# Kernel optimization log

Measured on AMD Instinct MI355X. Metric: run time of the kernel, lower is better.

## Reference

```python
import jax, jax.numpy as jnp
import numpy as np

B, N_NODES, T_IN = 512, 32, 12
HID, HEADS, OUT_CH, DEG = 64, 8, 9, 8


def setup_inputs() -> dict:
    key = jax.random.key(0)
    ks = jax.random.split(key, 26)
    rn = lambda k, s, sc=0.1: (jax.random.normal(k, s, jnp.float32) * sc)
    E = B * N_NODES * DEG
    src = jax.random.randint(ks[0], (E,), 0, N_NODES, jnp.int32)
    dst = jax.random.randint(ks[1], (E,), 0, N_NODES, jnp.int32)
    off = jnp.repeat(jnp.arange(B, dtype=jnp.int32) * N_NODES, N_NODES * DEG)
    edge_index = jnp.stack([src + off, dst + off])  # block-diagonal batched graph
    x = jax.random.normal(ks[2], (B, N_NODES, T_IN), jnp.float32)
    return {
        "x": x,
        "edge_index": edge_index,
        # gat1: in=T_IN -> HEADS*HID, concat
        "W1": rn(ks[3], (T_IN, HEADS * HID)),
        "a_src1": rn(ks[4], (HEADS, HID)),
        "a_dst1": rn(ks[5], (HEADS, HID)),
        "b1": rn(ks[6], (HEADS * HID,), 0.01),
        # gat2: in=HEADS*HID -> HID, heads=1, mean (concat=False)
        "W2": rn(ks[7], (HEADS * HID, HID), 0.05),
        "a_src2": rn(ks[8], (1, HID)),
        "a_dst2": rn(ks[9], (1, HID)),
        "b2": rn(ks[10], (HID,), 0.01),
        "gamma": jnp.ones((HID,), jnp.float32),
        "beta": jnp.zeros((HID,), jnp.float32),
        # gru1: input_size=N_NODES(=32), hidden=HID
        "Wi1": rn(ks[11], (3 * HID, N_NODES)),
        "Wh1": rn(ks[12], (3 * HID, HID)),
        "bi1": rn(ks[13], (3 * HID,), 0.01),
        "bh1": rn(ks[14], (3 * HID,), 0.01),
        # gru2: input_size=HID, hidden=HID
        "Wi2": rn(ks[15], (3 * HID, HID)),
        "Wh2": rn(ks[16], (3 * HID, HID)),
        "bi2": rn(ks[17], (3 * HID,), 0.01),
        "bh2": rn(ks[18], (3 * HID,), 0.01),
        "Wf": rn(ks[19], (OUT_CH, HID)),
        "bf": rn(ks[20], (OUT_CH,), 0.01),
    }


def _gat_layer(x, src, dst, W, a_s, a_d, b, concat):
    # PyG GATConv (eval mode, self-loops already appended by caller)
    Nn = x.shape[0]
    heads, hc = a_s.shape
    h = (x @ W).reshape(Nn, heads, hc)                 # [N, H, C]
    es = jnp.sum(h * a_s, axis=-1)                     # [N, H]
    ed = jnp.sum(h * a_d, axis=-1)
    e = jax.nn.leaky_relu(es[src] + ed[dst], 0.2)      # [E, H]
    m = jax.ops.segment_max(e, dst, num_segments=Nn)
    p = jnp.exp(e - m[dst])
    s = jax.ops.segment_sum(p, dst, num_segments=Nn)
    alpha = p / (s[dst] + 1e-16)                       # per-dst softmax
    out = jax.ops.segment_sum(h[src] * alpha[:, :, None], dst, num_segments=Nn)
    out = out.reshape(Nn, heads * hc) if concat else out.mean(axis=1)
    return out + b


def _gru(x, Wi, Wh, bi, bh):
    # torch.nn.GRU (batch_first) single layer; x: [B, T, F]
    H = Wh.shape[1]
    xi = x @ Wi.T + bi                                 # [B, T, 3H]
    def step(h, xt):
        gh = h @ Wh.T + bh
        r = jax.nn.sigmoid(xt[:, :H] + gh[:, :H])
        z = jax.nn.sigmoid(xt[:, H:2 * H] + gh[:, H:2 * H])
        n = jnp.tanh(xt[:, 2 * H:] + r * gh[:, 2 * H:])
        hn = (1.0 - z) * n + z * h
        return hn, hn
    h0 = jnp.zeros((x.shape[0], H), x.dtype)
    _, ys = jax.lax.scan(step, h0, jnp.swapaxes(xi, 0, 1))
    return jnp.swapaxes(ys, 0, 1)


def reference(x, edge_index, W1, a_src1, a_dst1, b1, W2, a_src2, a_dst2, b2,
              gamma, beta, Wi1, Wh1, bi1, bh1, Wi2, Wh2, bi2, bh2, Wf, bf):
    Bsz, Nn_, T = x.shape
    Nn = Bsz * Nn_
    xf = x.reshape(Nn, T)                              # dropout is identity in eval
    sl = jnp.arange(Nn, dtype=edge_index.dtype)        # PyG add_self_loops=True
    src = jnp.concatenate([edge_index[0], sl])
    dst = jnp.concatenate([edge_index[1], sl])
    h = jax.nn.elu(_gat_layer(xf, src, dst, W1, a_src1, a_dst1, b1, True))
    h = jax.nn.elu(_gat_layer(h, src, dst, W2, a_src2, a_dst2, b2, False))
    mu = h.mean(-1, keepdims=True)
    var = ((h - mu) ** 2).mean(-1, keepdims=True)
    h = (h - mu) / jnp.sqrt(var + 1e-5) * gamma + beta
    seq = h.reshape(Bsz, Nn_, -1).transpose(0, 2, 1)   # [B, HID(seq), N_NODES(feat)]
    g = _gru(seq, Wi1, Wh1, bi1, bh1)
    g = _gru(g, Wi2, Wh2, bi2, bh2)
    return g[:, -1, :] @ Wf.T + bf                     # [B, OUT_CH]
```

## Files before the change

### kernel.cpp

```cpp
#include <hip/hip_runtime.h>
#include <hip/hip_bf16.h>
#include <stdint.h>

#define BATCH 512
#define NN 32
#define T_IN 12
#define HID 64
#define HEADS 8
#define OUT_CH 9
#define EPB (NN*8)
#define ETOT (EPB+NN)
#define F1 (HEADS*HID)

using u16 = unsigned short;
using u32 = unsigned int;
typedef _Float16 f16;
typedef _Float16 f16x2 __attribute__((ext_vector_type(2)));
typedef u32 v4u __attribute__((ext_vector_type(4)));
typedef float v4f __attribute__((ext_vector_type(4)));

__device__ __forceinline__ float bf2f(u16 u){ return __uint_as_float(((u32)u)<<16); }
__device__ __forceinline__ u16 f2bf(float f){
    u32 x = __float_as_uint(f);
    u32 r = (x + 0x7FFFu + ((x>>16)&1u))>>16;
    return (u16)r;
}
__device__ __forceinline__ u32 packf16(float a, float b){
    f16x2 p; p.x=(f16)a; p.y=(f16)b; return __builtin_bit_cast(u32,p);
}
__device__ __forceinline__ u16 f2h16(float a){ f16 h=(f16)a; return __builtin_bit_cast(u16,h); }
__device__ __forceinline__ float h16f(u16 v){ f16 h=__builtin_bit_cast(f16,v); return (float)h; }
__device__ __forceinline__ float lof(u32 w){ return (float)__builtin_bit_cast(f16x2,w).x; }
__device__ __forceinline__ float hif(u32 w){ return (float)__builtin_bit_cast(f16x2,w).y; }
__device__ __forceinline__ float dot2(u32 a, u32 b, float c){
#if __has_builtin(__builtin_amdgcn_fdot2)
    return __builtin_amdgcn_fdot2(__builtin_bit_cast(f16x2,a), __builtin_bit_cast(f16x2,b), c, false);
#else
    return fmaf(lof(a),lof(b), fmaf(hif(a),hif(b), c));
#endif
}
__device__ __forceinline__ float elu1(float x){ return x > 0.f ? x : (__expf(x)-1.f); }
__device__ __forceinline__ float sigm(float x){ return 1.f/(1.f+__expf(-x)); }
__device__ __forceinline__ float tanh_(float x){ return 1.f - 2.f/(__expf(2.f*x)+1.f); }
__device__ __forceinline__ u32 fenc(float v){
    u32 b=__float_as_uint(v);
    return (b&0x80000000u) ? ~b : (b|0x80000000u);
}
__device__ __forceinline__ float fdec(u32 k){
    return __uint_as_float((k&0x80000000u) ? (k&0x7FFFFFFFu) : ~k);
}

#define DOT4(acc,A,W) do{ acc=dot2(A.x,W.x,acc); acc=dot2(A.y,W.y,acc); \
                          acc=dot2(A.z,W.z,acc); acc=dot2(A.w,W.w,acc); }while(0)
#define DOT32(acc,A0,A1,A2,A3,A4,A5,A6,A7,W0,W1,W2,W3,W4,W5,W6,W7) do{ \
    DOT4(acc,A0,W0); DOT4(acc,A1,W1); DOT4(acc,A2,W2); DOT4(acc,A3,W3); \
    DOT4(acc,A4,W4); DOT4(acc,A5,W5); DOT4(acc,A6,W6); DOT4(acc,A7,W7); }while(0)

__global__ __launch_bounds__(256) void k_detect(const u32* __restrict__ xw, int* __restrict__ flag){
    __shared__ int cnt;
    if(threadIdx.x==0) cnt=0;
    __syncthreads();
    int c=0;
    for(int i=threadIdx.x;i<4096;i+=256){
        u32 w=xw[i];
        if(w & 0x7FFFFFFFu){
            u32 el=(w>>7)&0xFFu;
            if(el>=0x90u) c++;
        }
    }
    atomicAdd(&cnt,c);
    __syncthreads();
    if(threadIdx.x==0) *flag = (cnt>256) ? 1 : 0;
}

struct CvtDesc {
    const void* src[16];
    void*       dst[16];
    int         n[16];
};

__global__ __launch_bounds__(256) void k_convert(CvtDesc d, const int* __restrict__ flag){
    const int seg = blockIdx.x;
    const int f = *flag;
    const void* s = d.src[seg];
    const int n = d.n[seg];
    const int stride = gridDim.y*256;
    float* o=(float*)d.dst[seg];
    for(int i=blockIdx.y*256+threadIdx.x;i<n;i+=stride)
        o[i] = f ? ((const float*)s)[i] : bf2f(((const u16*)s)[i]);
}

__global__ __launch_bounds__(256) void k_prep(
    const void* __restrict__ W2src, u16* __restrict__ W2i,
    const void* __restrict__ Wi1, const void* __restrict__ Wh1,
    const void* __restrict__ Wi2, const void* __restrict__ Wh2,
    u32* __restrict__ wpk, const int* __restrict__ flag)
{
    const int f=*flag;
    if(blockIdx.x<128){
        int i = blockIdx.x*256+threadIdx.x;
        int k=i>>6, j=i&63;
        float v = f? ((const float*)W2src)[i] : bf2f(((const u16*)W2src)[i]);
        W2i[ (((size_t)(k>>3)*64 + j)<<3) + (k&7) ] = f2h16(v);
    } else {
        int w = (blockIdx.x-128)*256+threadIdx.x;
        int m = w/6144;
        int rem = w - m*6144;
        int row = rem>>5, kw = rem&31;
        const void* s = (m==0)?Wi1 : (m==1)?Wh1 : (m==2)?Wi2 : Wh2;
        int K = (m==0)?32:64;
        int k0=2*kw, k1=k0+1;
        float v0=0.f, v1=0.f;
        if(k0<K) v0 = f? ((const float*)s)[row*K+k0] : bf2f(((const u16*)s)[row*K+k0]);
        if(k1<K) v1 = f? ((const float*)s)[row*K+k1] : bf2f(((const u16*)s)[row*K+k1]);
        wpk[w]=packf16(v0,v1);
    }
}

__global__ __launch_bounds__(256,2) void k_gat1(
    const float* __restrict__ x, const int* __restrict__ ei,
    const float* __restrict__ W1, const float* __restrict__ a_s, const float* __restrict__ a_d,
    const float* __restrict__ b1, u32* __restrict__ h1g)
{
    const int b = blockIdx.x, t = threadIdx.x;
    __shared__ __align__(16) float s_x[NN][12];
    __shared__ float s_W1[T_IN*F1];
    __shared__ __align__(16) u16 s_h[NN][520];
    __shared__ __align__(16) u32 s_aspk[HEADS*32], s_adpk[HEADS*32];
    __shared__ float s_es[NN][HEADS], s_ed[NN][HEADS];
    __shared__ unsigned char s_src[ETOT], s_dst[ETOT];
    __shared__ float s_al[HEADS][ETOT];
    __shared__ u32 s_mx[NN*HEADS];
    __shared__ float s_sm[NN*HEADS], s_inv[NN*HEADS];
    __shared__ int s_cnt[NN], s_off[NN], s_fil[NN];
    __shared__ short s_lst[ETOT];

    for(int i=t;i<NN*T_IN;i+=256) s_x[i/12][i%12] = x[b*NN*T_IN + i];
    for(int i=t;i<T_IN*F1;i+=256) s_W1[i]=W1[i];
    s_aspk[t]=packf16(a_s[2*t],a_s[2*t+1]);
    s_adpk[t]=packf16(a_d[2*t],a_d[2*t+1]);
    s_mx[t]=0u; s_sm[t]=0.f;
    if(t<EPB){
        s_src[t] = (unsigned char)(ei[b*EPB+t] - b*NN);
        s_dst[t] = (unsigned char)(ei[(size_t)BATCH*EPB + b*EPB+t] - b*NN);
    }
    if(t<NN){ s_src[EPB+t]=s_dst[EPB+t]=(unsigned char)t; s_cnt[t]=0; s_fil[t]=0; }
    __syncthreads();

    {
        v4f Wa0,Wa1,Wa2,Wb0,Wb1,Wb2;
        Wa0.x=s_W1[0*F1+t]; Wa0.y=s_W1[1*F1+t]; Wa0.z=s_W1[2*F1+t]; Wa0.w=s_W1[3*F1+t];
        Wa1.x=s_W1[4*F1+t]; Wa1.y=s_W1[5*F1+t]; Wa1.z=s_W1[6*F1+t]; Wa1.w=s_W1[7*F1+t];
        Wa2.x=s_W1[8*F1+t]; Wa2.y=s_W1[9*F1+t]; Wa2.z=s_W1[10*F1+t]; Wa2.w=s_W1[11*F1+t];
        Wb0.x=s_W1[0*F1+t+256]; Wb0.y=s_W1[1*F1+t+256]; Wb0.z=s_W1[2*F1+t+256]; Wb0.w=s_W1[3*F1+t+256];
        Wb1.x=s_W1[4*F1+t+256]; Wb1.y=s_W1[5*F1+t+256]; Wb1.z=s_W1[6*F1+t+256]; Wb1.w=s_W1[7*F1+t+256];
        Wb2.x=s_W1[8*F1+t+256]; Wb2.y=s_W1[9*F1+t+256]; Wb2.z=s_W1[10*F1+t+256]; Wb2.w=s_W1[11*F1+t+256];
        for(int n=0;n<NN;n++){
            const float4* xp=(const float4*)s_x[n];
            float4 xa=xp[0], xb=xp[1], xc=xp[2];
            float A=0.f,B=0.f;
            A=fmaf(xa.x,Wa0.x,A); A=fmaf(xa.y,Wa0.y,A); A=fmaf(xa.z,Wa0.z,A); A=fmaf(xa.w,Wa0.w,A);
            A=fmaf(xb.x,Wa1.x,A); A=fmaf(xb.y,Wa1.y,A); A=fmaf(xb.z,Wa1.z,A); A=fmaf(xb.w,Wa1.w,A);
            A=fmaf(xc.x,Wa2.x,A); A=fmaf(xc.y,Wa2.y,A); A=fmaf(xc.z,Wa2.z,A); A=fmaf(xc.w,Wa2.w,A);
            B=fmaf(xa.x,Wb0.x,B); B=fmaf(xa.y,Wb0.y,B); B=fmaf(xa.z,Wb0.z,B); B=fmaf(xa.w,Wb0.w,B);
            B=fmaf(xb.x,Wb1.x,B); B=fmaf(xb.y,Wb1.y,B); B=fmaf(xb.z,Wb1.z,B); B=fmaf(xb.w,Wb1.w,B);
            B=fmaf(xc.x,Wb2.x,B); B=fmaf(xc.y,Wb2.y,B); B=fmaf(xc.z,Wb2.z,B); B=fmaf(xc.w,Wb2.w,B);
            s_h[n][t]=f2h16(A); s_h[n][t+256]=f2h16(B);
        }
    }
    for(int e=t;e<ETOT;e+=256) atomicAdd(&s_cnt[s_dst[e]],1);
    __syncthreads();

    {
        int n=t&31, hd=t>>5;
        const v4u* hp=(const v4u*)((const u16*)s_h[n] + hd*64);
        v4u h0=hp[0],h1=hp[1],h2=hp[2],h3=hp[3],h4=hp[4],h5=hp[5],h6=hp[6],h7=hp[7];
        const v4u* ap=(const v4u*)&s_aspk[hd*32];
        const v4u* dp=(const v4u*)&s_adpk[hd*32];
        float e1=0.f,e2=0.f;
        { v4u w=ap[0]; DOT4(e1,h0,w); w=ap[1]; DOT4(e1,h1,w); w=ap[2]; DOT4(e1,h2,w); w=ap[3]; DOT4(e1,h3,w);
          w=ap[4]; DOT4(e1,h4,w); w=ap[5]; DOT4(e1,h5,w); w=ap[6]; DOT4(e1,h6,w); w=ap[7]; DOT4(e1,h7,w); }
        { v4u w=dp[0]; DOT4(e2,h0,w); w=dp[1]; DOT4(e2,h1,w); w=dp[2]; DOT4(e2,h2,w); w=dp[3]; DOT4(e2,h3,w);
          w=dp[4]; DOT4(e2,h4,w); w=dp[5]; DOT4(e2,h5,w); w=dp[6]; DOT4(e2,h6,w); w=dp[7]; DOT4(e2,h7,w); }
        s_es[n][hd]=e1; s_ed[n][hd]=e2;
    }
    if(t==0){ int o=0; for(int i=0;i<NN;i++){ s_off[i]=o; o+=s_cnt[i]; } }
    __syncthreads();

    for(int e=t;e<ETOT;e+=256){
        int d=s_dst[e]; int p=atomicAdd(&s_fil[d],1); s_lst[s_off[d]+p]=(short)e;
    }
    for(int i=t;i<ETOT*HEADS;i+=256){
        int hd=i/ETOT, e=i-hd*ETOT;
// ... 120 lines not shown
        }
        s_h2[n0+0][j0]=a00; s_h2[n0+0][j0+1]=a01;
        s_h2[n0+1][j0]=a10; s_h2[n0+1][j0+1]=a11;
        s_h2[n0+2][j0]=a20; s_h2[n0+2][j0+1]=a21;
        s_h2[n0+3][j0]=a30; s_h2[n0+3][j0+1]=a31;
    }
    __syncthreads();

    {
        int n=t>>3, g=t&7;
        float e1=0,e2=0;
        #pragma unroll
        for(int cc=0; cc<8; cc++){
            float hv = s_h2[n][g*8+cc];
            e1 += hv*a_s2[g*8+cc];
            e2 += hv*a_d2[g*8+cc];
        }
        #pragma unroll
        for(int m=1;m<8;m<<=1){ e1 += __shfl_xor(e1,m,64); e2 += __shfl_xor(e2,m,64); }
        if(g==0){ s_es[n]=e1; s_ed[n]=e2; }
    }
    if(t==0){ int o=0; for(int i=0;i<NN;i++){ s_off[i]=o; o+=s_cnt[i]; } }
    __syncthreads();

    for(int e=t;e<ETOT;e+=256){
        int d=s_dst[e]; int p=atomicAdd(&s_fil[d],1); s_lst[s_off[d]+p]=(short)e;
    }
    for(int e=t;e<ETOT;e+=256){
        int d=s_dst[e];
        float v = s_es[s_src[e]] + s_ed[d];
        v = v>0.f? v:0.2f*v;
        s_al[e]=v;
        atomicMax(&s_mx[d], fenc(v));
    }
    __syncthreads();

    for(int e=t;e<ETOT;e+=256){
        int d=s_dst[e];
        float p=__expf(s_al[e]-fdec(s_mx[d]));
        s_al[e]=p;
        atomicAdd(&s_sm[d], p);
    }
    __syncthreads();
    if(t<NN) s_inv[t]=1.f/(s_sm[t]+1e-16f);
    __syncthreads();

    {
        int n=t>>3, g=t&7;
        v4f a0=0, a1=0;
        int o=s_off[n], cnt=s_cnt[n];
        float inv=s_inv[n];
        for(int i=0;i<cnt;i++){
            int e=s_lst[o+i]; float a=s_al[e]; int sr=s_src[e];
            const float4* hp=(const float4*)&s_h2[sr][g*8];
            float4 v0=hp[0], v1=hp[1];
            a0.x=fmaf(a,v0.x,a0.x); a0.y=fmaf(a,v0.y,a0.y); a0.z=fmaf(a,v0.z,a0.z); a0.w=fmaf(a,v0.w,a0.w);
            a1.x=fmaf(a,v1.x,a1.x); a1.y=fmaf(a,v1.y,a1.y); a1.z=fmaf(a,v1.z,a1.z); a1.w=fmaf(a,v1.w,a1.w);
        }
        const float* bp=b2+g*8;
        float v0=elu1(a0.x*inv+bp[0]), v1=elu1(a0.y*inv+bp[1]);
        float v2=elu1(a0.z*inv+bp[2]), v3=elu1(a0.w*inv+bp[3]);
        float v4=elu1(a1.x*inv+bp[4]), v5=elu1(a1.y*inv+bp[5]);
        float v6=elu1(a1.z*inv+bp[6]), v7=elu1(a1.w*inv+bp[7]);
        float sum=v0+v1+v2+v3+v4+v5+v6+v7;
        float sq=v0*v0+v1*v1+v2*v2+v3*v3+v4*v4+v5*v5+v6*v6+v7*v7;
        #pragma unroll
        for(int m=1;m<8;m<<=1){ sum+=__shfl_xor(sum,m,64); sq+=__shfl_xor(sq,m,64); }
        float mu = sum*(1.f/64.f);
        float var = sq*(1.f/64.f) - mu*mu;
        float rs = rsqrtf(var + 1e-5f);
        float* outp = hlng + (size_t)b*HID*NN;
        int c=g*8;
        outp[(c+0)*NN+n]=(v0-mu)*rs*gam[c+0]+bet[c+0];
        outp[(c+1)*NN+n]=(v1-mu)*rs*gam[c+1]+bet[c+1];
        outp[(c+2)*NN+n]=(v2-mu)*rs*gam[c+2]+bet[c+2];
        outp[(c+3)*NN+n]=(v3-mu)*rs*gam[c+3]+bet[c+3];
        outp[(c+4)*NN+n]=(v4-mu)*rs*gam[c+4]+bet[c+4];
        outp[(c+5)*NN+n]=(v5-mu)*rs*gam[c+5]+bet[c+5];
        outp[(c+6)*NN+n]=(v6-mu)*rs*gam[c+6]+bet[c+6];
        outp[(c+7)*NN+n]=(v7-mu)*rs*gam[c+7]+bet[c+7];
    }
}

__global__ __launch_bounds__(256,1) void k_grum(
    const float* __restrict__ hlng, const u32* __restrict__ wpk,
    const float* __restrict__ bi1, const float* __restrict__ bh1,
    const float* __restrict__ bi2, const float* __restrict__ bh2,
    const float* __restrict__ Wf, const float* __restrict__ bfv,
    void* __restrict__ outp, const int* __restrict__ flag)
{
    const int b0=blockIdx.x*2, t=threadIdx.x;
    const int wave=t>>6, u=t&63;
    __shared__ __align__(16) u32 s_x[2][64*16];
    __shared__ __align__(16) u32 s_xi[2][64*96];
    __shared__ __align__(16) u32 s_y[2][64*32];
    __shared__ __align__(16) u32 s_h[2][32];
    __shared__ float s_hf[2][64];

    for(int w=t;w<2048;w+=256){
        int bb=w>>10, idx=w&1023;
        const float2* g=(const float2*)(hlng + (size_t)(b0+bb)*2048);
        float2 f=g[idx]; s_x[bb][idx]=packf16(f.x,f.y);
    }
    __syncthreads();

    for(int r=t;r<384;r+=256){
        int bb=r>=192, row=r-bb*192;
        const v4u* wr=(const v4u*)wpk + row*8;
        v4u w0=wr[0],w1=wr[1],w2=wr[2],w3=wr[3];
        float bias=bi1[row];
        u16* o=(u16*)s_xi[bb] + row;
        for(int step=0;step<64;step++){
            asm volatile("" : "+v"(w0),"+v"(w1),"+v"(w2),"+v"(w3));
            const v4u* xp=(const v4u*)&s_x[bb][step*16];
            v4u a0=xp[0],a1=xp[1],a2=xp[2],a3=xp[3];
            float a=bias;
            DOT4(a,a0,w0); DOT4(a,a1,w1); DOT4(a,a2,w2); DOT4(a,a3,w3);
            o[step*192]=f2h16(a);
        }
    }
    __syncthreads();

    if(wave<2){
        const int bb=wave;
        const v4u* wh=(const v4u*)(wpk + 6144);
        v4u r0=wh[u*8+0],r1=wh[u*8+1],r2=wh[u*8+2],r3=wh[u*8+3],
            r4=wh[u*8+4],r5=wh[u*8+5],r6=wh[u*8+6],r7=wh[u*8+7];
        v4u z0=wh[(64+u)*8+0],z1=wh[(64+u)*8+1],z2=wh[(64+u)*8+2],z3=wh[(64+u)*8+3],
            z4=wh[(64+u)*8+4],z5=wh[(64+u)*8+5],z6=wh[(64+u)*8+6],z7=wh[(64+u)*8+7];
        v4u n0=wh[(128+u)*8+0],n1=wh[(128+u)*8+1],n2=wh[(128+u)*8+2],n3=wh[(128+u)*8+3],
            n4=wh[(128+u)*8+4],n5=wh[(128+u)*8+5],n6=wh[(128+u)*8+6],n7=wh[(128+u)*8+7];
        float bhr=bh1[u], bhz=bh1[64+u], bhn=bh1[128+u];
        if(u<32) s_h[bb][u]=0u;
        float h=0.f;
        for(int st=0;st<64;st++){
            asm volatile("" : "+v"(r0),"+v"(r1),"+v"(r2),"+v"(r3),"+v"(r4),"+v"(r5),"+v"(r6),"+v"(r7),
                              "+v"(z0),"+v"(z1),"+v"(z2),"+v"(z3),"+v"(z4),"+v"(z5),"+v"(z6),"+v"(z7),
                              "+v"(n0),"+v"(n1),"+v"(n2),"+v"(n3),"+v"(n4),"+v"(n5),"+v"(n6),"+v"(n7));
            const u16* xr=(const u16*)s_xi[bb] + st*192;
            float xir=h16f(xr[u]), xiz=h16f(xr[64+u]), xin=h16f(xr[128+u]);
            const v4u* hp=(const v4u*)s_h[bb];
            v4u A0=hp[0],A1=hp[1],A2=hp[2],A3=hp[3],A4=hp[4],A5=hp[5],A6=hp[6],A7=hp[7];
            float gr=bhr,gz=bhz,gn=bhn;
            DOT32(gr,A0,A1,A2,A3,A4,A5,A6,A7,r0,r1,r2,r3,r4,r5,r6,r7);
            DOT32(gz,A0,A1,A2,A3,A4,A5,A6,A7,z0,z1,z2,z3,z4,z5,z6,z7);
            DOT32(gn,A0,A1,A2,A3,A4,A5,A6,A7,n0,n1,n2,n3,n4,n5,n6,n7);
            float rr=sigm(xir+gr), zz=sigm(xiz+gz);
            float nn=tanh_(xin + rr*gn);
            h=(1.f-zz)*nn+zz*h;
            u16 hv=f2h16(h);
            ((u16*)s_h[bb])[u]=hv;
            ((u16*)s_y[bb])[st*64+u]=hv;
        }
    }
    __syncthreads();

    for(int r=t;r<384;r+=256){
        int bb=r>=192, row=r-bb*192;
        const v4u* wr=(const v4u*)(wpk + 2*6144) + row*8;
        v4u w0=wr[0],w1=wr[1],w2=wr[2],w3=wr[3],w4=wr[4],w5=wr[5],w6=wr[6],w7=wr[7];
        float bias=bi2[row];
        u16* o=(u16*)s_xi[bb] + row;
        for(int step=0;step<64;step++){
            asm volatile("" : "+v"(w0),"+v"(w1),"+v"(w2),"+v"(w3),
                              "+v"(w4),"+v"(w5),"+v"(w6),"+v"(w7));
            const v4u* xp=(const v4u*)&s_y[bb][step*32];
            v4u a0=xp[0],a1=xp[1],a2=xp[2],a3=xp[3],a4=xp[4],a5=xp[5],a6=xp[6],a7=xp[7];
            float a=bias;
            DOT32(a,a0,a1,a2,a3,a4,a5,a6,a7,w0,w1,w2,w3,w4,w5,w6,w7);
            o[step*192]=f2h16(a);
        }
    }
    __syncthreads();

    if(wave<2){
        const int bb=wave;
        const v4u* wh=(const v4u*)(wpk + 3*6144);
        v4u r0=wh[u*8+0],r1=wh[u*8+1],r2=wh[u*8+2],r3=wh[u*8+3],
            r4=wh[u*8+4],r5=wh[u*8+5],r6=wh[u*8+6],r7=wh[u*8+7];
        v4u z0=wh[(64+u)*8+0],z1=wh[(64+u)*8+1],z2=wh[(64+u)*8+2],z3=wh[(64+u)*8+3],
            z4=wh[(64+u)*8+4],z5=wh[(64+u)*8+5],z6=wh[(64+u)*8+6],z7=wh[(64+u)*8+7];
        v4u n0=wh[(128+u)*8+0],n1=wh[(128+u)*8+1],n2=wh[(128+u)*8+2],n3=wh[(128+u)*8+3],
            n4=wh[(128+u)*8+4],n5=wh[(128+u)*8+5],n6=wh[(128+u)*8+6],n7=wh[(128+u)*8+7];
        float bhr=bh2[u], bhz=bh2[64+u], bhn=bh2[128+u];
        if(u<32) s_h[bb][u]=0u;
        float h=0.f;
        for(int st=0;st<64;st++){
            asm volatile("" : "+v"(r0),"+v"(r1),"+v"(r2),"+v"(r3),"+v"(r4),"+v"(r5),"+v"(r6),"+v"(r7),
                              "+v"(z0),"+v"(z1),"+v"(z2),"+v"(z3),"+v"(z4),"+v"(z5),"+v"(z6),"+v"(z7),
                              "+v"(n0),"+v"(n1),"+v"(n2),"+v"(n3),"+v"(n4),"+v"(n5),"+v"(n6),"+v"(n7));
            const u16* xr=(const u16*)s_xi[bb] + st*192;
            float xir=h16f(xr[u]), xiz=h16f(xr[64+u]), xin=h16f(xr[128+u]);
            const v4u* hp=(const v4u*)s_h[bb];
            v4u A0=hp[0],A1=hp[1],A2=hp[2],A3=hp[3],A4=hp[4],A5=hp[5],A6=hp[6],A7=hp[7];
            float gr=bhr,gz=bhz,gn=bhn;
            DOT32(gr,A0,A1,A2,A3,A4,A5,A6,A7,r0,r1,r2,r3,r4,r5,r6,r7);
            DOT32(gz,A0,A1,A2,A3,A4,A5,A6,A7,z0,z1,z2,z3,z4,z5,z6,z7);
            DOT32(gn,A0,A1,A2,A3,A4,A5,A6,A7,n0,n1,n2,n3,n4,n5,n6,n7);
            float rr=sigm(xir+gr), zz=sigm(xiz+gz);
            float nn=tanh_(xin + rr*gn);
            h=(1.f-zz)*nn+zz*h;
            ((u16*)s_h[bb])[u]=f2h16(h);
        }
        s_hf[bb][u]=h;
    }
    __syncthreads();

    if(t<2*OUT_CH){
        int bb=t/OUT_CH, o=t-bb*OUT_CH;
        float acc=bfv[o];
        const float4* wp=(const float4*)(Wf + o*64);
        const float4* hp=(const float4*)s_hf[bb];
        #pragma unroll
        for(int k=0;k<16;k++){
            float4 w=wp[k], v=hp[k];
            acc += w.x*v.x + w.y*v.y + w.z*v.z + w.w*v.w;
        }
        if(*flag) ((float*)outp)[(b0+bb)*OUT_CH+o]=acc;
        else      ((u16*)outp)[(b0+bb)*OUT_CH+o]=f2bf(acc);
    }
}

extern "C" void kernel_launch(void* const* d_in, const int* in_sizes, int n_in,
                              void* d_out, int out_size, void* d_ws, size_t ws_size,
                              hipStream_t stream)
{
    char* ws=(char*)d_ws;
    int* flag = (int*)ws;
    float* cf = (float*)(ws + 256);
    float* c_x   = cf; cf+=196608;
    float* c_W1  = cf; cf+=6144;
    float* c_as1 = cf; cf+=512;
    float* c_ad1 = cf; cf+=512;
    float* c_b1  = cf; cf+=512;
    float* c_as2 = cf; cf+=64;
    float* c_ad2 = cf; cf+=64;
    float* c_b2  = cf; cf+=64;
    float* c_gam = cf; cf+=64;
    float* c_bet = cf; cf+=64;
    float* c_bi1 = cf; cf+=192;
    float* c_bh1 = cf; cf+=192;
    float* c_bi2 = cf; cf+=192;
    float* c_bh2 = cf; cf+=192;
    float* c_Wf  = cf; cf+=576;
    float* c_bf  = cf; cf+=9;
    uintptr_t p = ((uintptr_t)cf + 255) & ~(uintptr_t)255;
    u16* c_W2i = (u16*)p;
    p = (p + 32768*2 + 255) & ~(uintptr_t)255;
    u32* wpk = (u32*)p;
    p = (p + 24576*4 + 255) & ~(uintptr_t)255;
    u32* h1g = (u32*)p;
    p = (p + (size_t)BATCH*NN*256*4 + 255) & ~(uintptr_t)255;
    float* hlng = (float*)p;

    const int* ei = (const int*)d_in[1];

    CvtDesc d;
    const int srcIdx[16] = {0,2,3,4,5,7,8,9,10,11,14,15,18,19,20,21};
    void* dsts[16] = {c_x,c_W1,c_as1,c_ad1,c_b1,c_as2,c_ad2,c_b2,c_gam,c_bet,
                      c_bi1,c_bh1,c_bi2,c_bh2,c_Wf,c_bf};
    const int ns[16] = {196608,6144,512,512,512,64,64,64,64,64,
                        192,192,192,192,576,9};
    for(int i=0;i<16;i++){ d.src[i]=d_in[srcIdx[i]]; d.dst[i]=dsts[i]; d.n[i]=ns[i]; }

    k_detect <<<dim3(1),dim3(256),0,stream>>>((const u32*)d_in[0], flag);
    k_convert<<<dim3(16,8),dim3(256),0,stream>>>(d, flag);
    k_prep   <<<dim3(224),dim3(256),0,stream>>>(d_in[6], c_W2i,
                                                d_in[12], d_in[13], d_in[16], d_in[17], wpk, flag);
    k_gat1   <<<dim3(BATCH),dim3(256),0,stream>>>(c_x,ei,c_W1,c_as1,c_ad1,c_b1,h1g);
    k_gat2ln <<<dim3(BATCH),dim3(256),0,stream>>>(h1g,ei,(const uint4*)c_W2i,c_as2,c_ad2,c_b2,c_gam,c_bet,hlng);
    k_grum   <<<dim3(BATCH/2),dim3(256),0,stream>>>(hlng, wpk, c_bi1,c_bh1,c_bi2,c_bh2,
                                                    c_Wf, c_bf, d_out, flag);
}
```

Measured before the change: 264.6 us.

## Run both GRU batch recurrences in one wave with hidden weights staged in LDS

```diff
diff --git a/kernel.cpp b/kernel.cpp
--- a/kernel.cpp
+++ b/kernel.cpp
@@ -404,9 +404,10 @@
 {
     const int b0=blockIdx.x*2, t=threadIdx.x;
     const int wave=t>>6, u=t&63;
-    __shared__ __align__(16) u32 s_x[2][64*16];
-    __shared__ __align__(16) u32 s_xi[2][64*96];
-    __shared__ __align__(16) u32 s_y[2][64*32];
+    __shared__ __align__(16) u32 s_x[2][1024];
+    __shared__ __align__(16) u16 s_xi[2][192*66];
+    __shared__ __align__(16) u32 s_y[2][2048];
+    __shared__ __align__(16) u32 s_w[6144];
     __shared__ __align__(16) u32 s_h[2][32];
     __shared__ float s_hf[2][64];
 
@@ -414,6 +415,10 @@
         int bb=w>>10, idx=w&1023;
         const float2* g=(const float2*)(hlng + (size_t)(b0+bb)*2048);
         float2 f=g[idx]; s_x[bb][idx]=packf16(f.x,f.y);
+    }
+    for(int i=t;i<6144;i+=256){
+        int gate=i>>11, rem=i&2047, kb=rem>>8, r2=rem&255, uu=r2>>2, j=r2&3;
+        s_w[i] = wpk[6144 + (gate*64+uu)*32 + kb*4 + j];
     }
     __syncthreads();
 
@@ -422,100 +427,103 @@
         const v4u* wr=(const v4u*)wpk + row*8;
         v4u w0=wr[0],w1=wr[1],w2=wr[2],w3=wr[3];
         float bias=bi1[row];
-        u16* o=(u16*)s_xi[bb] + row;
+        u16* o=&s_xi[bb][row*66];
         for(int step=0;step<64;step++){
-            asm volatile("" : "+v"(w0),"+v"(w1),"+v"(w2),"+v"(w3));
             const v4u* xp=(const v4u*)&s_x[bb][step*16];
             v4u a0=xp[0],a1=xp[1],a2=xp[2],a3=xp[3];
             float a=bias;
             DOT4(a,a0,w0); DOT4(a,a1,w1); DOT4(a,a2,w2); DOT4(a,a3,w3);
-            o[step*192]=f2h16(a);
-        }
-    }
-    __syncthreads();
-
-    if(wave<2){
-        const int bb=wave;
-        const v4u* wh=(const v4u*)(wpk + 6144);
-        v4u r0=wh[u*8+0],r1=wh[u*8+1],r2=wh[u*8+2],r3=wh[u*8+3],
-            r4=wh[u*8+4],r5=wh[u*8+5],r6=wh[u*8+6],r7=wh[u*8+7];
-        v4u z0=wh[(64+u)*8+0],z1=wh[(64+u)*8+1],z2=wh[(64+u)*8+2],z3=wh[(64+u)*8+3],
-            z4=wh[(64+u)*8+4],z5=wh[(64+u)*8+5],z6=wh[(64+u)*8+6],z7=wh[(64+u)*8+7];
-        v4u n0=wh[(128+u)*8+0],n1=wh[(128+u)*8+1],n2=wh[(128+u)*8+2],n3=wh[(128+u)*8+3],
-            n4=wh[(128+u)*8+4],n5=wh[(128+u)*8+5],n6=wh[(128+u)*8+6],n7=wh[(128+u)*8+7];
+            o[step]=f2h16(a);
+        }
+    }
+    __syncthreads();
+
+    if(wave==0){
+        if(u<32){ s_h[0][u]=0u; s_h[1][u]=0u; }
+        const v4u* wv=(const v4u*)s_w;
         float bhr=bh1[u], bhz=bh1[64+u], bhn=bh1[128+u];
-        if(u<32) s_h[bb][u]=0u;
-        float h=0.f;
+        float h0=0.f, h1=0.f;
+        const u16* x0r=&s_xi[0][u*66];
+        const u16* x0z=&s_xi[0][(64+u)*66];
+        const u16* x0n=&s_xi[0][(128+u)*66];
+        const u16* x1r=&s_xi[1][u*66];
+        const u16* x1z=&s_xi[1][(64+u)*66];
+        const u16* x1n=&s_xi[1][(128+u)*66];
         for(int st=0;st<64;st++){
-            asm volatile("" : "+v"(r0),"+v"(r1),"+v"(r2),"+v"(r3),"+v"(r4),"+v"(r5),"+v"(r6),"+v"(r7),
-                              "+v"(z0),"+v"(z1),"+v"(z2),"+v"(z3),"+v"(z4),"+v"(z5),"+v"(z6),"+v"(z7),
-                              "+v"(n0),"+v"(n1),"+v"(n2),"+v"(n3),"+v"(n4),"+v"(n5),"+v"(n6),"+v"(n7));
-            const u16* xr=(const u16*)s_xi[bb] + st*192;
-            float xir=h16f(xr[u]), xiz=h16f(xr[64+u]), xin=h16f(xr[128+u]);
-            const v4u* hp=(const v4u*)s_h[bb];
-            v4u A0=hp[0],A1=hp[1],A2=hp[2],A3=hp[3],A4=hp[4],A5=hp[5],A6=hp[6],A7=hp[7];
-            float gr=bhr,gz=bhz,gn=bhn;
-            DOT32(gr,A0,A1,A2,A3,A4,A5,A6,A7,r0,r1,r2,r3,r4,r5,r6,r7);
-            DOT32(gz,A0,A1,A2,A3,A4,A5,A6,A7,z0,z1,z2,z3,z4,z5,z6,z7);
-            DOT32(gn,A0,A1,A2,A3,A4,A5,A6,A7,n0,n1,n2,n3,n4,n5,n6,n7);
-            float rr=sigm(xir+gr), zz=sigm(xiz+gz);
-            float nn=tanh_(xin + rr*gn);
-            h=(1.f-zz)*nn+zz*h;
-            u16 hv=f2h16(h);
-            ((u16*)s_h[bb])[u]=hv;
-            ((u16*)s_y[bb])[st*64+u]=hv;
-        }
-    }
-    __syncthreads();
-
+            const v4u* hp0=(const v4u*)s_h[0];
+            const v4u* hp1=(const v4u*)s_h[1];
+            float gr0=bhr,gz0=bhz,gn0=bhn, gr1=bhr,gz1=bhz,gn1=bhn;
+            #pragma unroll
+            for(int kb=0;kb<8;kb++){
+                v4u wR=wv[kb*64+u], wZ=wv[512+kb*64+u], wN=wv[1024+kb*64+u];
+                v4u A=hp0[kb], B=hp1[kb];
+                DOT4(gr0,A,wR); DOT4(gz0,A,wZ); DOT4(gn0,A,wN);
+                DOT4(gr1,B,wR); DOT4(gz1,B,wZ); DOT4(gn1,B,wN);
+            }
+            float r0=sigm(h16f(x0r[st])+gr0), z0=sigm(h16f(x0z[st])+gz0);
+            float n0=tanh_(h16f(x0n[st]) + r0*gn0);
+            h0=(1.f-z0)*n0+z0*h0;
+            float r1=sigm(h16f(x1r[st])+gr1), z1=sigm(h16f(x1z[st])+gz1);
+            float n1=tanh_(h16f(x1n[st]) + r1*gn1);
+            h1=(1.f-z1)*n1+z1*h1;
+            u16 hv0=f2h16(h0), hv1=f2h16(h1);
+            ((u16*)s_h[0])[u]=hv0; ((u16*)s_h[1])[u]=hv1;
+            ((u16*)s_y[0])[st*64+u]=hv0; ((u16*)s_y[1])[st*64+u]=hv1;
+        }
+    }
+    __syncthreads();
+
+    for(int i=t;i<6144;i+=256){
+        int gate=i>>11, rem=i&2047, kb=rem>>8, r2=rem&255, uu=r2>>2, j=r2&3;
+        s_w[i] = wpk[3*6144 + (gate*64+uu)*32 + kb*4 + j];
+    }
     for(int r=t;r<384;r+=256){
         int bb=r>=192, row=r-bb*192;
         const v4u* wr=(const v4u*)(wpk + 2*6144) + row*8;
         v4u w0=wr[0],w1=wr[1],w2=wr[2],w3=wr[3],w4=wr[4],w5=wr[5],w6=wr[6],w7=wr[7];
         float bias=bi2[row];
-        u16* o=(u16*)s_xi[bb] + row;
+        u16* o=&s_xi[bb][row*66];
         for(int step=0;step<64;step++){
-            asm volatile("" : "+v"(w0),"+v"(w1),"+v"(w2),"+v"(w3),
-                              "+v"(w4),"+v"(w5),"+v"(w6),"+v"(w7));
             const v4u* xp=(const v4u*)&s_y[bb][step*32];
             v4u a0=xp[0],a1=xp[1],a2=xp[2],a3=xp[3],a4=xp[4],a5=xp[5],a6=xp[6],a7=xp[7];
             float a=bias;
             DOT32(a,a0,a1,a2,a3,a4,a5,a6,a7,w0,w1,w2,w3,w4,w5,w6,w7);
-            o[step*192]=f2h16(a);
-        }
-    }
-    __syncthreads();
-
-    if(wave<2){
-        const int bb=wave;
-        const v4u* wh=(const v4u*)(wpk + 3*6144);
-        v4u r0=wh[u*8+0],r1=wh[u*8+1],r2=wh[u*8+2],r3=wh[u*8+3],
-            r4=wh[u*8+4],r5=wh[u*8+5],r6=wh[u*8+6],r7=wh[u*8+7];
-        v4u z0=wh[(64+u)*8+0],z1=wh[(64+u)*8+1],z2=wh[(64+u)*8+2],z3=wh[(64+u)*8+3],
-            z4=wh[(64+u)*8+4],z5=wh[(64+u)*8+5],z6=wh[(64+u)*8+6],z7=wh[(64+u)*8+7];
-        v4u n0=wh[(128+u)*8+0],n1=wh[(128+u)*8+1],n2=wh[(128+u)*8+2],n3=wh[(128+u)*8+3],
-            n4=wh[(128+u)*8+4],n5=wh[(128+u)*8+5],n6=wh[(128+u)*8+6],n7=wh[(128+u)*8+7];
+            o[step]=f2h16(a);
+        }
+    }
+    __syncthreads();
+
+    if(wave==0){
+        if(u<32){ s_h[0][u]=0u; s_h[1][u]=0u; }
+        const v4u* wv=(const v4u*)s_w;
         float bhr=bh2[u], bhz=bh2[64+u], bhn=bh2[128+u];
-        if(u<32) s_h[bb][u]=0u;
-        float h=0.f;
+        float h0=0.f, h1=0.f;
+        const u16* x0r=&s_xi[0][u*66];
+        const u16* x0z=&s_xi[0][(64+u)*66];
+        const u16* x0n=&s_xi[0][(128+u)*66];
+        const u16* x1r=&s_xi[1][u*66];
+        const u16* x1z=&s_xi[1][(64+u)*66];
+        const u16* x1n=&s_xi[1][(128+u)*66];
         for(int st=0;st<64;st++){
-            asm volatile("" : "+v"(r0),"+v"(r1),"+v"(r2),"+v"(r3),"+v"(r4),"+v"(r5),"+v"(r6),"+v"(r7),
-                              "+v"(z0),"+v"(z1),"+v"(z2),"+v"(z3),"+v"(z4),"+v"(z5),"+v"(z6),"+v"(z7),
-                              "+v"(n0),"+v"(n1),"+v"(n2),"+v"(n3),"+v"(n4),"+v"(n5),"+v"(n6),"+v"(n7));
-            const u16* xr=(const u16*)s_xi[bb] + st*192;
-            float xir=h16f(xr[u]), xiz=h16f(xr[64+u]), xin=h16f(xr[128+u]);
-            const v4u* hp=(const v4u*)s_h[bb];
-            v4u A0=hp[0],A1=hp[1],A2=hp[2],A3=hp[3],A4=hp[4],A5=hp[5],A6=hp[6],A7=hp[7];
-            float gr=bhr,gz=bhz,gn=bhn;
-            DOT32(gr,A0,A1,A2,A3,A4,A5,A6,A7,r0,r1,r2,r3,r4,r5,r6,r7);
-            DOT32(gz,A0,A1,A2,A3,A4,A5,A6,A7,z0,z1,z2,z3,z4,z5,z6,z7);
-            DOT32(gn,A0,A1,A2,A3,A4,A5,A6,A7,n0,n1,n2,n3,n4,n5,n6,n7);
-            float rr=sigm(xir+gr), zz=sigm(xiz+gz);
-            float nn=tanh_(xin + rr*gn);
-            h=(1.f-zz)*nn+zz*h;
-            ((u16*)s_h[bb])[u]=f2h16(h);
-        }
-        s_hf[bb][u]=h;
+            const v4u* hp0=(const v4u*)s_h[0];
+            const v4u* hp1=(const v4u*)s_h[1];
+            float gr0=bhr,gz0=bhz,gn0=bhn, gr1=bhr,gz1=bhz,gn1=bhn;
+            #pragma unroll
+            for(int kb=0;kb<8;kb++){
+                v4u wR=wv[kb*64+u], wZ=wv[512+kb*64+u], wN=wv[1024+kb*64+u];
+                v4u A=hp0[kb], B=hp1[kb];
+                DOT4(gr0,A,wR); DOT4(gz0,A,wZ); DOT4(gn0,A,wN);
+                DOT4(gr1,B,wR); DOT4(gz1,B,wZ); DOT4(gn1,B,wN);
+            }
+            float r0=sigm(h16f(x0r[st])+gr0), z0=sigm(h16f(x0z[st])+gz0);
+            float n0=tanh_(h16f(x0n[st]) + r0*gn0);
+            h0=(1.f-z0)*n0+z0*h0;
+            float r1=sigm(h16f(x1r[st])+gr1), z1=sigm(h16f(x1z[st])+gz1);
+            float n1=tanh_(h16f(x1n[st]) + r1*gn1);
+            h1=(1.f-z1)*n1+z1*h1;
+            ((u16*)s_h[0])[u]=f2h16(h0); ((u16*)s_h[1])[u]=f2h16(h1);
+        }
+        s_hf[0][u]=h0; s_hf[1][u]=h1;
     }
     __syncthreads();
 
```

After: 301.5 us. +13.9%, slower.

## Pipeline two GRU layers wavefront-style in one block and fuse setup kernels

Applied to the files above, without the earlier changes.

```diff
diff --git a/kernel.cpp b/kernel.cpp
--- a/kernel.cpp
+++ b/kernel.cpp
@@ -52,11 +52,20 @@
 
 #define DOT4(acc,A,W) do{ acc=dot2(A.x,W.x,acc); acc=dot2(A.y,W.y,acc); \
                           acc=dot2(A.z,W.z,acc); acc=dot2(A.w,W.w,acc); }while(0)
-#define DOT32(acc,A0,A1,A2,A3,A4,A5,A6,A7,W0,W1,W2,W3,W4,W5,W6,W7) do{ \
-    DOT4(acc,A0,W0); DOT4(acc,A1,W1); DOT4(acc,A2,W2); DOT4(acc,A3,W3); \
-    DOT4(acc,A4,W4); DOT4(acc,A5,W5); DOT4(acc,A6,W6); DOT4(acc,A7,W7); }while(0)
-
-__global__ __launch_bounds__(256) void k_detect(const u32* __restrict__ xw, int* __restrict__ flag){
+
+struct CvtDesc {
+    const void* src[16];
+    void*       dst[16];
+    int         n[16];
+};
+
+__global__ __launch_bounds__(256) void k_setup(
+    const u32* __restrict__ xw, CvtDesc d,
+    const void* __restrict__ W2src, u16* __restrict__ W2i,
+    const void* __restrict__ Wi1, const void* __restrict__ Wh1,
+    const void* __restrict__ Wi2, const void* __restrict__ Wh2,
+    u32* __restrict__ wpk, int* __restrict__ flag)
+{
     __shared__ int cnt;
     if(threadIdx.x==0) cnt=0;
     __syncthreads();
@@ -70,45 +79,29 @@
     }
     atomicAdd(&cnt,c);
     __syncthreads();
-    if(threadIdx.x==0) *flag = (cnt>256) ? 1 : 0;
-}
-
-struct CvtDesc {
-    const void* src[16];
-    void*       dst[16];
-    int         n[16];
-};
-
-__global__ __launch_bounds__(256) void k_convert(CvtDesc d, const int* __restrict__ flag){
-    const int seg = blockIdx.x;
-    const int f = *flag;
-    const void* s = d.src[seg];
-    const int n = d.n[seg];
-    const int stride = gridDim.y*256;
-    float* o=(float*)d.dst[seg];
-    for(int i=blockIdx.y*256+threadIdx.x;i<n;i+=stride)
-        o[i] = f ? ((const float*)s)[i] : bf2f(((const u16*)s)[i]);
-}
-
-__global__ __launch_bounds__(256) void k_prep(
-    const void* __restrict__ W2src, u16* __restrict__ W2i,
-    const void* __restrict__ Wi1, const void* __restrict__ Wh1,
-    const void* __restrict__ Wi2, const void* __restrict__ Wh2,
-    u32* __restrict__ wpk, const int* __restrict__ flag)
-{
-    const int f=*flag;
-    if(blockIdx.x<128){
-        int i = blockIdx.x*256+threadIdx.x;
+    const int f = (cnt>256) ? 1 : 0;
+    if(blockIdx.x==0 && threadIdx.x==0) *flag=f;
+
+    const int bk=blockIdx.x;
+    if(bk<128){
+        int seg=bk>>3, sub=bk&7;
+        const void* s=d.src[seg];
+        float* o=(float*)d.dst[seg];
+        int n=d.n[seg];
+        for(int i=sub*256+threadIdx.x;i<n;i+=2048)
+            o[i] = f ? ((const float*)s)[i] : bf2f(((const u16*)s)[i]);
+    } else if(bk<256){
+        int i=(bk-128)*256+threadIdx.x;
         int k=i>>6, j=i&63;
         float v = f? ((const float*)W2src)[i] : bf2f(((const u16*)W2src)[i]);
         W2i[ (((size_t)(k>>3)*64 + j)<<3) + (k&7) ] = f2h16(v);
     } else {
-        int w = (blockIdx.x-128)*256+threadIdx.x;
-        int m = w/6144;
-        int rem = w - m*6144;
-        int row = rem>>5, kw = rem&31;
-        const void* s = (m==0)?Wi1 : (m==1)?Wh1 : (m==2)?Wi2 : Wh2;
-        int K = (m==0)?32:64;
+        int w=(bk-256)*256+threadIdx.x;
+        int m=w/6144;
+        int rem=w-m*6144;
+        int row=rem>>5, kw=rem&31;
+        const void* s=(m==0)?Wi1:(m==1)?Wh1:(m==2)?Wi2:Wh2;
+        int K=(m==0)?32:64;
         int k0=2*kw, k1=k0+1;
         float v0=0.f, v1=0.f;
         if(k0<K) v0 = f? ((const float*)s)[row*K+k0] : bf2f(((const u16*)s)[row*K+k0]);
@@ -395,142 +388,117 @@
     }
 }
 
-__global__ __launch_bounds__(256,1) void k_grum(
+__global__ __launch_bounds__(256,2) void k_gruf(
     const float* __restrict__ hlng, const u32* __restrict__ wpk,
     const float* __restrict__ bi1, const float* __restrict__ bh1,
     const float* __restrict__ bi2, const float* __restrict__ bh2,
     const float* __restrict__ Wf, const float* __restrict__ bfv,
     void* __restrict__ outp, const int* __restrict__ flag)
 {
-    const int b0=blockIdx.x*2, t=threadIdx.x;
-    const int wave=t>>6, u=t&63;
-    __shared__ __align__(16) u32 s_x[2][64*16];
-    __shared__ __align__(16) u32 s_xi[2][64*96];
-    __shared__ __align__(16) u32 s_y[2][64*32];
-    __shared__ __align__(16) u32 s_h[2][32];
-    __shared__ float s_hf[2][64];
-
-    for(int w=t;w<2048;w+=256){
-        int bb=w>>10, idx=w&1023;
-        const float2* g=(const float2*)(hlng + (size_t)(b0+bb)*2048);
-        float2 f=g[idx]; s_x[bb][idx]=packf16(f.x,f.y);
-    }
-    __syncthreads();
-
-    for(int r=t;r<384;r+=256){
-        int bb=r>=192, row=r-bb*192;
-        const v4u* wr=(const v4u*)wpk + row*8;
-        v4u w0=wr[0],w1=wr[1],w2=wr[2],w3=wr[3];
-        float bias=bi1[row];
-        u16* o=(u16*)s_xi[bb] + row;
-        for(int step=0;step<64;step++){
-            asm volatile("" : "+v"(w0),"+v"(w1),"+v"(w2),"+v"(w3));
-            const v4u* xp=(const v4u*)&s_x[bb][step*16];
-            v4u a0=xp[0],a1=xp[1],a2=xp[2],a3=xp[3];
-            float a=bias;
-            DOT4(a,a0,w0); DOT4(a,a1,w1); DOT4(a,a2,w2); DOT4(a,a3,w3);
-            o[step*192]=f2h16(a);
-        }
-    }
-    __syncthreads();
-
-    if(wave<2){
-        const int bb=wave;
-        const v4u* wh=(const v4u*)(wpk + 6144);
-        v4u r0=wh[u*8+0],r1=wh[u*8+1],r2=wh[u*8+2],r3=wh[u*8+3],
-            r4=wh[u*8+4],r5=wh[u*8+5],r6=wh[u*8+6],r7=wh[u*8+7];
-        v4u z0=wh[(64+u)*8+0],z1=wh[(64+u)*8+1],z2=wh[(64+u)*8+2],z3=wh[(64+u)*8+3],
-            z4=wh[(64+u)*8+4],z5=wh[(64+u)*8+5],z6=wh[(64+u)*8+6],z7=wh[(64+u)*8+7];
-        v4u n0=wh[(128+u)*8+0],n1=wh[(128+u)*8+1],n2=wh[(128+u)*8+2],n3=wh[(128+u)*8+3],
-            n4=wh[(128+u)*8+4],n5=wh[(128+u)*8+5],n6=wh[(128+u)*8+6],n7=wh[(128+u)*8+7];
-        float bhr=bh1[u], bhz=bh1[64+u], bhn=bh1[128+u];
-        if(u<32) s_h[bb][u]=0u;
-        float h=0.f;
-        for(int st=0;st<64;st++){
-            asm volatile("" : "+v"(r0),"+v"(r1),"+v"(r2),"+v"(r3),"+v"(r4),"+v"(r5),"+v"(r6),"+v"(r7),
-                              "+v"(z0),"+v"(z1),"+v"(z2),"+v"(z3),"+v"(z4),"+v"(z5),"+v"(z6),"+v"(z7),
-                              "+v"(n0),"+v"(n1),"+v"(n2),"+v"(n3),"+v"(n4),"+v"(n5),"+v"(n6),"+v"(n7));
-            const u16* xr=(const u16*)s_xi[bb] + st*192;
-            float xir=h16f(xr[u]), xiz=h16f(xr[64+u]), xin=h16f(xr[128+u]);
-            const v4u* hp=(const v4u*)s_h[bb];
-            v4u A0=hp[0],A1=hp[1],A2=hp[2],A3=hp[3],A4=hp[4],A5=hp[5],A6=hp[6],A7=hp[7];
-            float gr=bhr,gz=bhz,gn=bhn;
-            DOT32(gr,A0,A1,A2,A3,A4,A5,A6,A7,r0,r1,r2,r3,r4,r5,r6,r7);
-            DOT32(gz,A0,A1,A2,A3,A4,A5,A6,A7,z0,z1,z2,z3,z4,z5,z6,z7);
-            DOT32(gn,A0,A1,A2,A3,A4,A5,A6,A7,n0,n1,n2,n3,n4,n5,n6,n7);
-            float rr=sigm(xir+gr), zz=sigm(xiz+gz);
-            float nn=tanh_(xin + rr*gn);
-            h=(1.f-zz)*nn+zz*h;
-            u16 hv=f2h16(h);
-            ((u16*)s_h[bb])[u]=hv;
-            ((u16*)s_y[bb])[st*64+u]=hv;
-        }
-    }
-    __syncthreads();
-
-    for(int r=t;r<384;r+=256){
-        int bb=r>=192, row=r-bb*192;
-        const v4u* wr=(const v4u*)(wpk + 2*6144) + row*8;
-        v4u w0=wr[0],w1=wr[1],w2=wr[2],w3=wr[3],w4=wr[4],w5=wr[5],w6=wr[6],w7=wr[7];
-        float bias=bi2[row];
-        u16* o=(u16*)s_xi[bb] + row;
-        for(int step=0;step<64;step++){
-            asm volatile("" : "+v"(w0),"+v"(w1),"+v"(w2),"+v"(w3),
-                              "+v"(w4),"+v"(w5),"+v"(w6),"+v"(w7));
-            const v4u* xp=(const v4u*)&s_y[bb][step*32];
-            v4u a0=xp[0],a1=xp[1],a2=xp[2],a3=xp[3],a4=xp[4],a5=xp[5],a6=xp[6],a7=xp[7];
-            float a=bias;
-            DOT32(a,a0,a1,a2,a3,a4,a5,a6,a7,w0,w1,w2,w3,w4,w5,w6,w7);
-            o[step*192]=f2h16(a);
-        }
-    }
-    __syncthreads();
-
-    if(wave<2){
-        const int bb=wave;
-        const v4u* wh=(const v4u*)(wpk + 3*6144);
-        v4u r0=wh[u*8+0],r1=wh[u*8+1],r2=wh[u*8+2],r3=wh[u*8+3],
-            r4=wh[u*8+4],r5=wh[u*8+5],r6=wh[u*8+6],r7=wh[u*8+7];
-        v4u z0=wh[(64+u)*8+0],z1=wh[(64+u)*8+1],z2=wh[(64+u)*8+2],z3=wh[(64+u)*8+3],
-            z4=wh[(64+u)*8+4],z5=wh[(64+u)*8+5],z6=wh[(64+u)*8+6],z7=wh[(64+u)*8+7];
-        v4u n0=wh[(128+u)*8+0],n1=wh[(128+u)*8+1],n2=wh[(128+u)*8+2],n3=wh[(128+u)*8+3],
-            n4=wh[(128+u)*8+4],n5=wh[(128+u)*8+5],n6=wh[(128+u)*8+6],n7=wh[(128+u)*8+7];
-        float bhr=bh2[u], bhz=bh2[64+u], bhn=bh2[128+u];
-        if(u<32) s_h[bb][u]=0u;
-        float h=0.f;
-        for(int st=0;st<64;st++){
-            asm volatile("" : "+v"(r0),"+v"(r1),"+v"(r2),"+v"(r3),"+v"(r4),"+v"(r5),"+v"(r6),"+v"(r7),
-                              "+v"(z0),"+v"(z1),"+v"(z2),"+v"(z3),"+v"(z4),"+v"(z5),"+v"(z6),"+v"(z7),
-                              "+v"(n0),"+v"(n1),"+v"(n2),"+v"(n3),"+v"(n4),"+v"(n5),"+v"(n6),"+v"(n7));
-            const u16* xr=(const u16*)s_xi[bb] + st*192;
-            float xir=h16f(xr[u]), xiz=h16f(xr[64+u]), xin=h16f(xr[128+u]);
-            const v4u* hp=(const v4u*)s_h[bb];
-            v4u A0=hp[0],A1=hp[1],A2=hp[2],A3=hp[3],A4=hp[4],A5=hp[5],A6=hp[6],A7=hp[7];
-            float gr=bhr,gz=bhz,gn=bhn;
-            DOT32(gr,A0,A1,A2,A3,A4,A5,A6,A7,r0,r1,r2,r3,r4,r5,r6,r7);
-            DOT32(gz,A0,A1,A2,A3,A4,A5,A6,A7,z0,z1,z2,z3,z4,z5,z6,z7);
-            DOT32(gn,A0,A1,A2,A3,A4,A5,A6,A7,n0,n1,n2,n3,n4,n5,n6,n7);
-            float rr=sigm(xir+gr), zz=sigm(xiz+gz);
-            float nn=tanh_(xin + rr*gn);
-            h=(1.f-zz)*nn+zz*h;
-            ((u16*)s_h[bb])[u]=f2h16(h);
-        }
-        s_hf[bb][u]=h;
-    }
-    __syncthreads();
-
-    if(t<2*OUT_CH){
-        int bb=t/OUT_CH, o=t-bb*OUT_CH;
-        float acc=bfv[o];
-        const float4* wp=(const float4*)(Wf + o*64);
-        const float4* hp=(const float4*)s_hf[bb];
+    const int b=blockIdx.x, t=threadIdx.x;
+    const int wave=t>>6, lane=t&63;
+    const int layer=wave>>1;
+    const int ublk=wave&1;
+    const int uu=lane&31, s=lane>>5;
+    const int u=ublk*32+uu;
+
+    __shared__ __align__(16) u32 s_x1[64*16];
+    __shared__ __align__(16) u32 s_h1[2][32];
+    __shared__ __align__(16) u32 s_h2[2][32];
+    __shared__ float s_h2f[64];
+
+    { const float2* g=(const float2*)(hlng + (size_t)b*2048);
+      for(int w=t;w<1024;w+=256){ float2 v=g[w]; s_x1[w]=packf16(v.x,v.y); } }
+    if(t<32){ s_h1[0][t]=0u; s_h1[1][t]=0u; s_h2[0][t]=0u; s_h2[1][t]=0u; }
+
+    u32 wiR[16],wiZ[16],wiN[16],whR[16],whZ[16],whN[16];
+    const u32* wiu = wpk + (size_t)(layer*2+0)*6144;
+    const u32* whu = wpk + (size_t)(layer*2+1)*6144;
+    if(layer==0){
+        #pragma unroll
+        for(int k=0;k<8;k++){
+            wiR[k]=wiu[u*32+s*8+k];
+            wiZ[k]=wiu[(64+u)*32+s*8+k];
+            wiN[k]=wiu[(128+u)*32+s*8+k];
+        }
+        #pragma unroll
+        for(int k=0;k<16;k++){
+            whR[k]=whu[u*32+s*16+k];
+            whZ[k]=whu[(64+u)*32+s*16+k];
+            whN[k]=whu[(128+u)*32+s*16+k];
+        }
+    } else {
+        #pragma unroll
+        for(int k=0;k<16;k++){
+            wiR[k]=wiu[u*32+s*16+k];
+            wiZ[k]=wiu[(64+u)*32+s*16+k];
+            wiN[k]=wiu[(128+u)*32+s*16+k];
+            whR[k]=whu[u*32+s*16+k];
+            whZ[k]=whu[(64+u)*32+s*16+k];
+            whN[k]=whu[(128+u)*32+s*16+k];
+        }
+    }
+    const float* bi = layer? bi2:bi1;
+    const float* bh = layer? bh2:bh1;
+    float br=bi[u]+bh[u], bz=bi[64+u]+bh[64+u], bxn=bi[128+u], bhn=bh[128+u];
+    float h=0.f;
+    __syncthreads();
+
+    for(int it=0; it<=64; ++it){
+        const int pb=(it-1)&1, cb=it&1;
+        bool act;
+        float pr=0.f,pz=0.f,pxn=0.f,phn=0.f;
+        if(layer==0){
+            act=(it<64);
+            if(act){
+                const u32* xp=&s_x1[it*16+s*8];
+                const u32* hp=&s_h1[pb][s*16];
+                #pragma unroll
+                for(int k=0;k<8;k++){ u32 xv=xp[k]; pr=dot2(xv,wiR[k],pr); pz=dot2(xv,wiZ[k],pz); pxn=dot2(xv,wiN[k],pxn); }
+                #pragma unroll
+                for(int k=0;k<16;k++){ u32 hv=hp[k]; pr=dot2(hv,whR[k],pr); pz=dot2(hv,whZ[k],pz); phn=dot2(hv,whN[k],phn); }
+            }
+        } else {
+            act=(it>=1);
+            if(act){
+                const u32* xp=&s_h1[pb][s*16];
+                const u32* hp=&s_h2[pb][s*16];
+                #pragma unroll
+                for(int k=0;k<16;k++){
+                    u32 xv=xp[k], hv=hp[k];
+                    pr=dot2(xv,wiR[k],pr); pz=dot2(xv,wiZ[k],pz); pxn=dot2(xv,wiN[k],pxn);
+                    pr=dot2(hv,whR[k],pr); pz=dot2(hv,whZ[k],pz); phn=dot2(hv,whN[k],phn);
+                }
+            }
+        }
+        if(act){
+            pr  += __shfl_xor(pr ,32,64);
+            pz  += __shfl_xor(pz ,32,64);
+            pxn += __shfl_xor(pxn,32,64);
+            phn += __shfl_xor(phn,32,64);
+            float r=sigm(pr+br), z=sigm(pz+bz);
+            float n=tanh_(pxn+bxn + r*(phn+bhn));
+            h=(1.f-z)*n + z*h;
+            if(s==0){
+                u16 hv=f2h16(h);
+                if(layer==0) ((u16*)s_h1[cb])[u]=hv;
+                else { ((u16*)s_h2[cb])[u]=hv; if(it==64) s_h2f[u]=h; }
+            }
+        }
+        __syncthreads();
+    }
+
+    if(t<OUT_CH){
+        float acc=bfv[t];
+        const float4* wp=(const float4*)(Wf + t*64);
+        const float4* hp=(const float4*)s_h2f;
         #pragma unroll
         for(int k=0;k<16;k++){
             float4 w=wp[k], v=hp[k];
             acc += w.x*v.x + w.y*v.y + w.z*v.z + w.w*v.w;
         }
-        if(*flag) ((float*)outp)[(b0+bb)*OUT_CH+o]=acc;
-        else      ((u16*)outp)[(b0+bb)*OUT_CH+o]=f2bf(acc);
+        if(*flag) ((float*)outp)[b*OUT_CH+t]=acc;
+        else      ((u16*)outp)[b*OUT_CH+t]=f2bf(acc);
     }
 }
 
@@ -576,12 +544,12 @@
                         192,192,192,192,576,9};
     for(int i=0;i<16;i++){ d.src[i]=d_in[srcIdx[i]]; d.dst[i]=dsts[i]; d.n[i]=ns[i]; }
 
-    k_detect <<<dim3(1),dim3(256),0,stream>>>((const u32*)d_in[0], flag);
-    k_convert<<<dim3(16,8),dim3(256),0,stream>>>(d, flag);
-    k_prep   <<<dim3(224),dim3(256),0,stream>>>(d_in[6], c_W2i,
-                                                d_in[12], d_in[13], d_in[16], d_in[17], wpk, flag);
+    k_setup  <<<dim3(352),dim3(256),0,stream>>>((const u32*)d_in[0], d,
+                                                d_in[6], c_W2i,
+                                                d_in[12], d_in[13], d_in[16], d_in[17],
+                                                wpk, flag);
     k_gat1   <<<dim3(BATCH),dim3(256),0,stream>>>(c_x,ei,c_W1,c_as1,c_ad1,c_b1,h1g);
     k_gat2ln <<<dim3(BATCH),dim3(256),0,stream>>>(h1g,ei,(const uint4*)c_W2i,c_as2,c_ad2,c_b2,c_gam,c_bet,hlng);
-    k_grum   <<<dim3(BATCH/2),dim3(256),0,stream>>>(hlng, wpk, c_bi1,c_bh1,c_bi2,c_bh2,
-                                                    c_Wf, c_bf, d_out, flag);
-}
+    k_gruf   <<<dim3(BATCH),dim3(256),0,stream>>>(hlng, wpk, c_bi1,c_bh1,c_bi2,c_bh2,
+                                                  c_Wf, c_bf, d_out, flag);
+}
```

After: 239.5 us. 9.5% less time.
